# Kernel optimization log

Measured on AMD Instinct MI355X. Metric: run time of the kernel, lower is better.

Reference implementation:

```python
import jax, jax.numpy as jnp
import numpy as np

B, C, H, W = 4, 256, 96, 96
FOUT = 32
HW = H * W
N = HW // 2  # inside/outside pixel counts (50/50 mask)


def setup_inputs() -> dict:
    key = jax.random.key(0)
    ks = jax.random.split(key, 6)
    f = jax.random.normal(ks[0], (B, C, H, W), dtype=jnp.float32)
    # deterministic alternating mask -> fixed N_in = N_out = HW/2 (jit-friendly)
    flat = (jnp.arange(HW) % 2).astype(jnp.float32)
    mask = jnp.broadcast_to(flat.reshape(1, 1, H, W), (B, 1, H, W))
    idx_in = jnp.nonzero(flat > 0.5, size=N)[0].astype(jnp.int32)   # mask == 1
    idx_out = jnp.nonzero(flat < 0.5, size=N)[0].astype(jnp.int32)  # mask == 0
    scale = 0.02
    Wq = jax.random.normal(ks[1], (FOUT, C), dtype=jnp.float32) * scale
    Wk = jax.random.normal(ks[2], (FOUT, C), dtype=jnp.float32) * scale
    Wv = jax.random.normal(ks[3], (C, C), dtype=jnp.float32) * scale
    bq = jnp.zeros((FOUT,), jnp.float32)
    bk = jnp.zeros((FOUT,), jnp.float32)
    bv = jnp.zeros((C,), jnp.float32)
    gamma = jax.random.uniform(ks[4], (1,), dtype=jnp.float32) + 0.25  # nonzero
    return {"f": f, "mask": mask, "idx_out": idx_out, "idx_in": idx_in,
            "Wq": Wq, "bq": bq, "Wk": Wk, "bk": bk, "Wv": Wv, "bv": bv,
            "gamma": gamma}


def reference(f, mask, idx_out, idx_in, Wq, bq, Wk, bk, Wv, bv, gamma):
    b, c, h, w = f.shape
    ff = f.reshape(b, c, h * w)              # (b, c, hw)
    f_out_pix = ff[:, :, idx_out]            # (b, c, Nout) gather outside pixels
    f_in_pix = ff[:, :, idx_in]              # (b, c, Nin)  gather inside pixels
    # 1x1 convs on gathered pixel sets == per-pixel linear projections
    q = jnp.einsum('oc,bcn->bon', Wq, f_out_pix) + bq[None, :, None]  # (b, fout, Nout)
    k = jnp.einsum('oc,bcn->bon', Wk, f_in_pix) + bk[None, :, None]   # (b, fout, Nin)
    v = jnp.einsum('dc,bcn->bdn', Wv, f_in_pix) + bv[None, :, None]   # (b, c, Nin)
    energy = jnp.einsum('boq,bok->bqk', q, k)       # (b, Nout, Nin)
    att = jax.nn.softmax(energy, axis=-1)
    r_v = jnp.einsum('bck,bqk->bcq', v, att)        # (b, c, Nout)
    ff2 = ff.at[:, :, idx_out].set(r_v)             # scatter write-back
    f_reshape = ff2.reshape(b, c, h, w)
    # NOTE: in torch, f_in aliases f's storage and is mutated by the scatter,
    # so f_in == f_reshape here. Reproduce that aliasing faithfully.
    f_out = f_reshape * (1.0 - mask) * gamma + f_reshape
    return (f_reshape, f_out)
```

## Files before the change

kernel.cpp:

```cpp
#include <hip/hip_runtime.h>
#include <math.h>

#define B_DIM    4
#define C_DIM    256
#define HW_DIM   9216
#define N_PIX    4608
#define FOUT_DIM 32
#define L2E      1.44269504f

typedef float  f32x4  __attribute__((ext_vector_type(4)));
typedef short  bf16x8 __attribute__((ext_vector_type(8)));

static __device__ __forceinline__ unsigned short f2bf(float x) {
    union { float f; unsigned int u; } v; v.f = x;
    unsigned int r = v.u + 0x7fffu + ((v.u >> 16) & 1u);
    return (unsigned short)(r >> 16);
}
static __device__ __forceinline__ float bf2f(unsigned short u) {
    union { unsigned int u; float f; } v; v.u = (unsigned int)u << 16; return v.f;
}

static __device__ __forceinline__ void gload_lds16(const unsigned short* g, unsigned short* l) {
    __builtin_amdgcn_global_load_lds(
        (const __attribute__((address_space(1))) void*)g,
        (__attribute__((address_space(3))) void*)l, 16, 0, 0);
}

__global__ __launch_bounds__(256) void gather_f(
    const float* __restrict__ f, const int* __restrict__ idx_out, const int* __restrict__ idx_in,
    unsigned short* __restrict__ Fo, unsigned short* __restrict__ Fi) {
    __shared__ float Fs[2][32][65];
    __shared__ int io[64], ii[64];
    const int t = threadIdx.x;
    const int n0 = blockIdx.x * 64, c0 = blockIdx.y * 32, b = blockIdx.z;
    if (t < 64) { io[t] = idx_out[n0 + t]; ii[t] = idx_in[n0 + t]; }
    __syncthreads();
    const float* fb = f + (size_t)b * C_DIM * HW_DIM;
    const int nn = t & 63, cg = t >> 6;
#pragma unroll
    for (int i = 0; i < 8; i++) {
        int c = cg * 8 + i;
        Fs[0][c][nn] = fb[(size_t)(c0 + c) * HW_DIM + io[nn]];
        Fs[1][c][nn] = fb[(size_t)(c0 + c) * HW_DIM + ii[nn]];
    }
    __syncthreads();
    {
        const int n = t >> 2, oc = (t & 3) * 8;
        size_t o = ((size_t)(b * N_PIX + n0 + n)) * C_DIM + c0 + oc;
        unsigned short tmp0[8], tmp1[8];
#pragma unroll
        for (int j = 0; j < 8; j++) {
            tmp0[j] = f2bf(Fs[0][oc + j][n]);
            tmp1[j] = f2bf(Fs[1][oc + j][n]);
        }
        *(uint4*)(Fo + o) = *(uint4*)tmp0;
        *(uint4*)(Fi + o) = *(uint4*)tmp1;
    }
}

#define FSP 40
__global__ __launch_bounds__(256) void prep(
    const unsigned short* __restrict__ Fo, const unsigned short* __restrict__ Fi,
    const float* __restrict__ Wq, const float* __restrict__ bq,
    const float* __restrict__ Wk, const float* __restrict__ bk,
    const float* __restrict__ Wv, const float* __restrict__ bv,
    unsigned short* __restrict__ Q, unsigned short* __restrict__ K,
    unsigned short* __restrict__ VT,
    const int* __restrict__ idx_out, const int* __restrict__ idx_in,
    int* __restrict__ inv) {
    __shared__ __align__(16) unsigned short SM[18688];
    const int bid = blockIdx.x, t = threadIdx.x;
    if (bid < 144) {
        unsigned short* Ws = SM;
        unsigned short* Fs = SM + 8448;
        const int n0 = (bid % 18) * 256, sel = (bid / 18) & 1, b = bid / 36;
        const unsigned short* FX = sel ? Fi : Fo;
        const float* W    = sel ? Wk : Wq;
        const float* bias = sel ? bk : bq;
        unsigned short* O = sel ? K : Q;
#pragma unroll
        for (int j = 0; j < 8; j++) {
            int fid = j * 256 + t, row = fid >> 6, f4 = fid & 63;
            float4 wv = *(const float4*)(W + (size_t)row * C_DIM + f4 * 4);
            uint2 pk;
            pk.x = f2bf(wv.x) | ((unsigned)f2bf(wv.y) << 16);
            pk.y = f2bf(wv.z) | ((unsigned)f2bf(wv.w) << 16);
            *(uint2*)(Ws + row * 264 + f4 * 4) = pk;
        }
        const int w = t >> 6, l = t & 63, lq = l & 15, lg = l >> 4;
        f32x4 acc[8];
#pragma unroll
        for (int i = 0; i < 8; i++) acc[i] = (f32x4){0.f, 0.f, 0.f, 0.f};
        for (int cs = 0; cs < 8; cs++) {
            __syncthreads();
#pragma unroll
            for (int j = 0; j < 4; j++) {
                int cid = j * 256 + t, row = cid >> 2, ch = cid & 3;
                *(uint4*)(Fs + row * FSP + ch * 8) =
                    *(const uint4*)(FX + ((size_t)(b * N_PIX + n0 + row)) * C_DIM + cs * 32 + ch * 8);
            }
            __syncthreads();
            bf16x8 bfr[2];
#pragma unroll
            for (int ob = 0; ob < 2; ob++)
                bfr[ob] = *(const bf16x8*)(Ws + (ob * 16 + lq) * 264 + cs * 32 + lg * 8);
#pragma unroll
            for (int ab = 0; ab < 4; ab++) {
                bf16x8 a = *(const bf16x8*)(Fs + (w * 64 + ab * 16 + lq) * FSP + lg * 8);
#pragma unroll
                for (int ob = 0; ob < 2; ob++)
                    acc[ab * 2 + ob] = __builtin_amdgcn_mfma_f32_16x16x32_bf16(a, bfr[ob], acc[ab * 2 + ob], 0, 0, 0);
            }
        }
#pragma unroll
        for (int ab = 0; ab < 4; ab++)
#pragma unroll
            for (int ob = 0; ob < 2; ob++)
#pragma unroll
                for (int r = 0; r < 4; r++) {
                    int n = n0 + w * 64 + ab * 16 + lg * 4 + r;
                    int o = ob * 16 + lq;
                    O[((size_t)(b * N_PIX + n)) * FOUT_DIM + o] = f2bf(acc[ab * 2 + ob][r] + bias[o]);
                }
    } else if (bid < 432) {
        unsigned short* Ws = SM;
        unsigned short* Fs = SM + 5120;
        const int vb = bid - 144;
        const int n0 = (vb % 36) * 128, d0 = ((vb / 36) & 1) * 128, b = vb / 72;
        const int w = t >> 6, wd = w & 1, wn = w >> 1, l = t & 63, lq = l & 15, lg = l >> 4;
        f32x4 acc[16];
#pragma unroll
        for (int i = 0; i < 16; i++) acc[i] = (f32x4){0.f, 0.f, 0.f, 0.f};
        for (int cs = 0; cs < 8; cs++) {
            __syncthreads();
#pragma unroll
            for (int j = 0; j < 4; j++) {
                int row = j * 32 + (t >> 3), f4 = t & 7;
                float4 wv = *(const float4*)(Wv + (size_t)(d0 + row) * C_DIM + cs * 32 + f4 * 4);
                uint2 pk;
                pk.x = f2bf(wv.x) | ((unsigned)f2bf(wv.y) << 16);
                pk.y = f2bf(wv.z) | ((unsigned)f2bf(wv.w) << 16);
                *(uint2*)(Ws + row * FSP + f4 * 4) = pk;
            }
#pragma unroll
            for (int j = 0; j < 2; j++) {
                int cid = j * 256 + t, row = cid >> 2, ch = cid & 3;
                *(uint4*)(Fs + row * FSP + ch * 8) =
                    *(const uint4*)(Fi + ((size_t)(b * N_PIX + n0 + row)) * C_DIM + cs * 32 + ch * 8);
            }
            __syncthreads();
            bf16x8 bfr[4];
#pragma unroll
            for (int nb = 0; nb < 4; nb++)
                bfr[nb] = *(const bf16x8*)(Fs + (wn * 64 + nb * 16 + lq) * FSP + lg * 8);
#pragma unroll
            for (int ab = 0; ab < 4; ab++) {
                bf16x8 a = *(const bf16x8*)(Ws + (wd * 64 + ab * 16 + lq) * FSP + lg * 8);
#pragma unroll
                for (int nb = 0; nb < 4; nb++)
                    acc[ab * 4 + nb] = __builtin_amdgcn_mfma_f32_16x16x32_bf16(a, bfr[nb], acc[ab * 4 + nb], 0, 0, 0);
            }
        }
#pragma unroll
        for (int ab = 0; ab < 4; ab++)
#pragma unroll
            for (int r = 0; r < 4; r++) {
                int d = d0 + wd * 64 + ab * 16 + lg * 4 + r;
                float bvv = bv[d];
#pragma unroll
                for (int nb = 0; nb < 4; nb++) {
                    int n = n0 + wn * 64 + nb * 16 + lq;
                    VT[((size_t)(b * C_DIM + d)) * N_PIX + n] = f2bf(acc[ab * 4 + nb][r] + bvv);
                }
            }
    } else {
        int i = (bid - 432) * 256 + t;
        if (i < N_PIX) {
            inv[idx_out[i]] = i;
            inv[idx_in[i]] = -1;
        }
    }
}

__global__ __launch_bounds__(256, 2) void flash_attn(
    const unsigned short* __restrict__ Q, const unsigned short* __restrict__ K,
    const unsigned short* __restrict__ VT,
    unsigned short* __restrict__ Rpart, float* __restrict__ lpart) {
    __shared__ __align__(16) unsigned short VB[256 * 64];
    __shared__ __align__(16) unsigned short PB[2][32 * 72];
    __shared__ float lred[2][2][2][16];
    const int t = threadIdx.x, w = t >> 6, l = t & 63, lq = l & 15, lg = l >> 4;
    const int qg = w & 1, dh = w >> 1;
    const int bid = blockIdx.x;
    const int bz = bid & 7, b = bz & 3, ks = bz >> 2;
    const int q0 = (bid >> 3) * 64 + qg * 32;
    const int d0 = dh * 128;
    const unsigned short* Qb = Q + (size_t)b * N_PIX * FOUT_DIM;
    const unsigned short* Kb = K + (size_t)b * N_PIX * FOUT_DIM;
    const unsigned short* Vb = VT + (size_t)b * C_DIM * N_PIX;
    unsigned short* Rp = Rpart + (size_t)ks * 4718592;
    float* lp = lpart + ks * (B_DIM * N_PIX);

    bf16x8 qfr[2];
    qfr[0] = *(const bf16x8*)(Qb + (size_t)(q0 + lq) * 32 + lg * 8);
    qfr[1] = *(const bf16x8*)(Qb + (size_t)(q0 + 16 + lq) * 32 + lg * 8);

    f32x4 acc[2][8];
#pragma unroll
    for (int qb = 0; qb < 2; qb++)
#pragma unroll
        for (int db = 0; db < 8; db++) acc[qb][db] = (f32x4){0.f, 0.f, 0.f, 0.f};
    float lsum[2] = {0.f, 0.f};

    int voff[8];
#pragma unroll
    for (int j = 0; j < 8; j++) {
        int row = (w * 8 + j) * 8 + (l >> 3);
        int ch  = (l & 7) ^ (row & 7);
        voff[j] = row * N_PIX + ch * 8;
    }
    const int kt0 = ks * 36;
    bf16x8 kpf[2];
    {
        int kg = kt0 * 64;
#pragma unroll
        for (int j = 0; j < 8; j++)
            gload_lds16(Vb + voff[j] + kg, VB + (w * 8 + j) * 512);
#pragma unroll
        for (int kb = 0; kb < 2; kb++)
            kpf[kb] = *(const bf16x8*)(Kb + (size_t)(kg + dh * 32 + kb * 16 + lq) * 32 + lg * 8);
    }

    const int swz = lq & 7;
#pragma unroll 1
    for (int it = 0; it < 36; it++) {
        {
            const f32x4 z4 = {0.f, 0.f, 0.f, 0.f};
#pragma unroll
            for (int qb = 0; qb < 2; qb++) {
                f32x4 s[2];
#pragma unroll
                for (int kb = 0; kb < 2; kb++)
                    s[kb] = __builtin_amdgcn_mfma_f32_16x16x32_bf16(kpf[kb], qfr[qb], z4, 0, 0, 0);
                float ps = 0.f;
#pragma unroll
                for (int kb = 0; kb < 2; kb++) {
                    float p0 = exp2f(s[kb][0] * L2E);
                    float p1 = exp2f(s[kb][1] * L2E);
                    float p2 = exp2f(s[kb][2] * L2E);
                    float p3 = exp2f(s[kb][3] * L2E);
                    ps += (p0 + p1) + (p2 + p3);
                    unsigned int u0 = (__float_as_uint(p0) + 0x8000u) >> 16;
                    unsigned int u1 = (__float_as_uint(p1) + 0x8000u) & 0xffff0000u;
                    unsigned int u2 = (__float_as_uint(p2) + 0x8000u) >> 16;
                    unsigned int u3 = (__float_as_uint(p3) + 0x8000u) & 0xffff0000u;
                    uint2 pk; pk.x = u0 | u1; pk.y = u2 | u3;
                    *(uint2*)(PB[qg] + (qb * 16 + lq) * 72 + dh * 32 + kb * 16 + lg * 4) = pk;
                }
                lsum[qb] += ps;
            }
        }
        __syncthreads();
        if (it + 1 < 36) {
            int kn = (kt0 + it + 1) * 64;
#pragma unroll
            for (int kb = 0; kb < 2; kb++)
                kpf[kb] = *(const bf16x8*)(Kb + (size_t)(kn + dh * 32 + kb * 16 + lq) * 32 + lg * 8);
        }
        bf16x8 af[2][2];
#pragma unroll
        for (int qb = 0; qb < 2; qb++) {
            af[qb][0] = *(const bf16x8*)(PB[qg] + (qb * 16 + lq) * 72 + lg * 8);
            af[qb][1] = *(const bf16x8*)(PB[qg] + (qb * 16 + lq) * 72 + 32 + lg * 8);
        }
#pragma unroll
        for (int db = 0; db < 8; db++) {
            int row = d0 + db * 16 + lq;
            bf16x8 b0 = *(const bf16x8*)(VB + row * 64 + (lg ^ swz) * 8);
            bf16x8 b1 = *(const bf16x8*)(VB + row * 64 + ((lg + 4) ^ swz) * 8);
#pragma unroll
            for (int qb = 0; qb < 2; qb++) {
                acc[qb][db] = __builtin_amdgcn_mfma_f32_16x16x32_bf16(af[qb][0], b0, acc[qb][db], 0, 0, 0);
                acc[qb][db] = __builtin_amdgcn_mfma_f32_16x16x32_bf16(af[qb][1], b1, acc[qb][db], 0, 0, 0);
            }
        }
        __syncthreads();
        if (it + 1 < 36) {
            int kn = (kt0 + it + 1) * 64;
#pragma unroll
            for (int j = 0; j < 8; j++)
                gload_lds16(Vb + voff[j] + kn, VB + (w * 8 + j) * 512);
        }
    }
#pragma unroll
    for (int qb = 0; qb < 2; qb++)
#pragma unroll
        for (int r = 0; r < 4; r++) {
            int q = q0 + qb * 16 + lg * 4 + r;
            unsigned short* rp = Rp + ((size_t)(b * N_PIX + q)) * C_DIM + d0;
#pragma unroll
            for (int db = 0; db < 8; db++)
                rp[db * 16 + lq] = f2bf(acc[qb][db][r]);
        }
#pragma unroll
    for (int qb = 0; qb < 2; qb++) {
        float v = lsum[qb];
        v += __shfl_xor(v, 16);
        v += __shfl_xor(v, 32);
        if (l < 16) lred[dh][qg][qb][l] = v;
    }
    __syncthreads();
    if (dh == 0 && l < 16) {
#pragma unroll
        for (int qb = 0; qb < 2; qb++)
            lp[b * N_PIX + q0 + qb * 16 + l] = lred[0][qg][qb][l] + lred[1][qg][qb][l];
    }
}

__global__ __launch_bounds__(256) void epilogue(
    const float* __restrict__ f, const float* __restrict__ mask,
    const unsigned short* __restrict__ R0, const unsigned short* __restrict__ R1,
    const float* __restrict__ l0, const float* __restrict__ l1,
    const int* __restrict__ inv, const float* __restrict__ gamma,
    float* __restrict__ out0, float* __restrict__ out1) {
    const int gid = blockIdx.x * 256 + threadIdx.x;
    const size_t e = (size_t)gid * 4;
    const int p = (int)(e % HW_DIM);
    const int bc = (int)(e / HW_DIM);
    const int b = bc >> 8;
    const int c = bc & 255;
    const float g = gamma[0];
    float4 fv = *(const float4*)(f + e);
    const float* fvp = (const float*)&fv;
    float o0[4], o1[4];
#pragma unroll
    for (int u = 0; u < 4; u++) {
        int pp = p + u;
        int n = inv[pp];
        float val;
        if (n >= 0) {
            size_t ri = ((size_t)(b * N_PIX + n)) * C_DIM + c;
            float s = bf2f(R0[ri]) + bf2f(R1[ri]);
            val = s / (l0[b * N_PIX + n] + l1[b * N_PIX + n]);
        } else {
            val = fvp[u];
        }
        float mv = mask[b * HW_DIM + pp];
        o0[u] = val;
        o1[u] = val * (1.0f + g * (1.0f - mv));
    }
    *(float4*)(out0 + e) = make_float4(o0[0], o0[1], o0[2], o0[3]);
    *(float4*)(out1 + e) = make_float4(o1[0], o1[1], o1[2], o1[3]);
}

extern "C" void kernel_launch(void* const* d_in, const int* in_sizes, int n_in,
                              void* d_out, int out_size, void* d_ws, size_t ws_size,
                              hipStream_t stream) {
    const float* f       = (const float*)d_in[0];
    const float* mask    = (const float*)d_in[1];
    const int*   idx_out = (const int*)d_in[2];
    const int*   idx_in  = (const int*)d_in[3];
    const float* Wq      = (const float*)d_in[4];
    const float* bq      = (const float*)d_in[5];
    const float* Wk      = (const float*)d_in[6];
    const float* bk      = (const float*)d_in[7];
    const float* Wv      = (const float*)d_in[8];
    const float* bv      = (const float*)d_in[9];
    const float* gamma   = (const float*)d_in[10];

    unsigned short* ws   = (unsigned short*)d_ws;
    unsigned short* Fo   = ws;
    unsigned short* Fi   = ws + 4718592;
    unsigned short* VTw  = ws + 9437184;
    unsigned short* Qw   = ws + 14155776;
    unsigned short* Kw   = ws + 14745600;
    float*          lptr = (float*)(ws + 15335424);
    int*            inv  = (int*)(lptr + 2 * B_DIM * N_PIX);
    unsigned short* Rpart = Fo;

    float* out0 = (float*)d_out;
    float* out1 = out0 + (size_t)B_DIM * C_DIM * HW_DIM;

    gather_f<<<dim3(72, 8, B_DIM), dim3(256), 0, stream>>>(f, idx_out, idx_in, Fo, Fi);
    prep<<<dim3(450), dim3(256), 0, stream>>>(Fo, Fi, Wq, bq, Wk, bk, Wv, bv,
                                              Qw, Kw, VTw, idx_out, idx_in, inv);
    flash_attn<<<dim3(576), dim3(256), 0, stream>>>(Qw, Kw, VTw, Rpart, lptr);
    epilogue<<<dim3(9216), dim3(256), 0, stream>>>(f, mask, Rpart, Rpart + 4718592,
                                                   lptr, lptr + B_DIM * N_PIX, inv, gamma, out0, out1);
}
```

Measured before the change: 268.4 us.

## Stage attention output tiles in LDS for coalesced epilogue transpose

The epilogue now processes a 32-pixel block across all channels. It first loads each pixel's bf16 R rows from both partial buffers into shared memory with 16-byte coalesced loads, then writes outputs in channel-major order from LDS. This replaces the strided per-element gathers of R and the per-element divides with one reciprocal per pixel. The cost is extra shared memory, two barriers, and possible LDS bank conflicts on the transposed reads.

```diff
diff --git a/kernel.cpp b/kernel.cpp
--- a/kernel.cpp
+++ b/kernel.cpp
@@ -323,34 +323,65 @@
     const float* __restrict__ l0, const float* __restrict__ l1,
     const int* __restrict__ inv, const float* __restrict__ gamma,
     float* __restrict__ out0, float* __restrict__ out1) {
-    const int gid = blockIdx.x * 256 + threadIdx.x;
-    const size_t e = (size_t)gid * 4;
-    const int p = (int)(e % HW_DIM);
-    const int bc = (int)(e / HW_DIM);
-    const int b = bc >> 8;
-    const int c = bc & 255;
+    __shared__ __align__(16) unsigned short Rs0[32][264];
+    __shared__ __align__(16) unsigned short Rs1[32][264];
+    __shared__ int nns[32];
+    __shared__ float lr[32];
+    const int t = threadIdx.x, bid = blockIdx.x;
+    const int b = bid / 288, p0 = (bid % 288) * 32;
+    if (t < 32) {
+        int n = inv[p0 + t];
+        nns[t] = n;
+        if (n >= 0) lr[t] = 1.0f / (l0[b * N_PIX + n] + l1[b * N_PIX + n]);
+    }
+    __syncthreads();
+    {
+        const int s = t >> 3, j = t & 7;
+        int n = nns[s];
+        if (n >= 0) {
+            const unsigned short* r0 = R0 + ((size_t)(b * N_PIX + n)) * C_DIM;
+            const unsigned short* r1 = R1 + ((size_t)(b * N_PIX + n)) * C_DIM;
+#pragma unroll
+            for (int k = 0; k < 4; k++) {
+                int ch = j + k * 8;
+                *(uint4*)(&Rs0[s][ch * 8]) = *(const uint4*)(r0 + ch * 8);
+                *(uint4*)(&Rs1[s][ch * 8]) = *(const uint4*)(r1 + ch * 8);
+            }
+        }
+    }
+    __syncthreads();
     const float g = gamma[0];
-    float4 fv = *(const float4*)(f + e);
-    const float* fvp = (const float*)&fv;
-    float o0[4], o1[4];
+    const int cg = t >> 3, po = (t & 7) * 4;
+    float4 mv4 = *(const float4*)(mask + (size_t)b * HW_DIM + p0 + po);
+    const float* mvp = (const float*)&mv4;
+    int ns[4]; float lrv[4];
 #pragma unroll
     for (int u = 0; u < 4; u++) {
-        int pp = p + u;
-        int n = inv[pp];
-        float val;
-        if (n >= 0) {
-            size_t ri = ((size_t)(b * N_PIX + n)) * C_DIM + c;
-            float s = bf2f(R0[ri]) + bf2f(R1[ri]);
-            val = s / (l0[b * N_PIX + n] + l1[b * N_PIX + n]);
-        } else {
-            val = fvp[u];
-        }
-        float mv = mask[b * HW_DIM + pp];
-        o0[u] = val;
-        o1[u] = val * (1.0f + g * (1.0f - mv));
-    }
-    *(float4*)(out0 + e) = make_float4(o0[0], o0[1], o0[2], o0[3]);
-    *(float4*)(out1 + e) = make_float4(o1[0], o1[1], o1[2], o1[3]);
+        ns[u] = nns[po + u];
+        lrv[u] = (ns[u] >= 0) ? lr[po + u] : 0.f;
+    }
+#pragma unroll
+    for (int i = 0; i < 8; i++) {
+        const int c = cg * 8 + i;
+        const size_t e = ((size_t)(b * C_DIM + c)) * HW_DIM + p0 + po;
+        float4 fv = *(const float4*)(f + e);
+        const float* fvp = (const float*)&fv;
+        float o0[4], o1[4];
+#pragma unroll
+        for (int u = 0; u < 4; u++) {
+            float val;
+            if (ns[u] >= 0) {
+                int s = po + u;
+                val = (bf2f(Rs0[s][c]) + bf2f(Rs1[s][c])) * lrv[u];
+            } else {
+                val = fvp[u];
+            }
+            o0[u] = val;
+            o1[u] = val * (1.0f + g * (1.0f - mvp[u]));
+        }
+        *(float4*)(out0 + e) = make_float4(o0[0], o0[1], o0[2], o0[3]);
+        *(float4*)(out1 + e) = make_float4(o1[0], o1[1], o1[2], o1[3]);
+    }
 }
 
 extern "C" void kernel_launch(void* const* d_in, const int* in_sizes, int n_in,
@@ -385,6 +416,6 @@
     prep<<<dim3(450), dim3(256), 0, stream>>>(Fo, Fi, Wq, bq, Wk, bk, Wv, bv,
                                               Qw, Kw, VTw, idx_out, idx_in, inv);
     flash_attn<<<dim3(576), dim3(256), 0, stream>>>(Qw, Kw, VTw, Rpart, lptr);
-    epilogue<<<dim3(9216), dim3(256), 0, stream>>>(f, mask, Rpart, Rpart + 4718592,
+    epilogue<<<dim3(1152), dim3(256), 0, stream>>>(f, mask, Rpart, Rpart + 4718592,
                                                    lptr, lptr + B_DIM * N_PIX, inv, gamma, out0, out1);
 }
```

New measurement: 234.8 us. 12.5% less time.
